# Optimization experiments

Hardware: AMD Instinct MI355X
Metric: run time of the kernel (lower is better)

Reference implementation:

```python
import jax, jax.numpy as jnp
import numpy as np

B, D_IN, T = 8, 1024, 2048
K, D_CB = 8192, 8
COMMIT = 0.005
CB_LOSS_W = 1.0
EPS = 1e-12  # F.normalize eps


def _wn(v, g):
    # torch weight_norm(dim=0) on a 1x1 Conv1d: w = g * v / ||v|| per output row
    return g[:, None] * v / jnp.linalg.norm(v, axis=1, keepdims=True)


def _l2n(x):
    return x / jnp.maximum(jnp.linalg.norm(x, axis=-1, keepdims=True), EPS)


def setup_inputs() -> dict:
    key = jax.random.key(0)
    ks = jax.random.split(key, 8)
    return {
        "z": jax.random.normal(ks[0], (B, D_IN, T), dtype=jnp.float32),
        "in_v": jax.random.normal(ks[1], (D_CB, D_IN), dtype=jnp.float32) * 0.02,
        "in_g": jnp.ones((D_CB,), dtype=jnp.float32),
        "in_b": jnp.zeros((D_CB,), dtype=jnp.float32),
        "out_v": jax.random.normal(ks[2], (D_IN, D_CB), dtype=jnp.float32) * 0.02,
        "out_g": jnp.ones((D_IN,), dtype=jnp.float32),
        "out_b": jnp.zeros((D_IN,), dtype=jnp.float32),
        "codebook": jax.random.normal(ks[3], (K, D_CB), dtype=jnp.float32),
    }


def reference(z, in_v, in_g, in_b, out_v, out_g, out_b, codebook):
    sg = jax.lax.stop_gradient
    # in_project: weight-normed 1x1 conv == matmul over channel dim
    w_in = _wn(in_v, in_g)
    z_e = jnp.einsum('oi,bit->bot', w_in, z) + in_b[None, :, None]  # [B, D_CB, T]

    # decode_latents
    enc = jnp.transpose(z_e, (0, 2, 1)).reshape(-1, D_CB)  # (B*T, D_CB)
    enc_n = _l2n(enc)
    cb_n = _l2n(codebook)
    dist = (jnp.sum(enc_n**2, axis=1, keepdims=True)
            - 2.0 * enc_n @ cb_n.T
            + jnp.sum(cb_n**2, axis=1)[None, :])  # (B*T, K)
    indices = jnp.argmin(dist, axis=1).reshape(B, T)  # [B, T]
    z_q = jnp.transpose(codebook[indices], (0, 2, 1))  # [B, D_CB, T] (unnormalized codebook)

    # training losses (per-batch means over (d, t))
    commit_loss = jnp.mean((z_e - sg(z_q)) ** 2, axis=(1, 2)) * COMMIT
    codebook_loss = jnp.mean((z_q - sg(z_e)) ** 2, axis=(1, 2)) * CB_LOSS_W

    # straight-through estimator
    z_q_st = z_e + sg(z_q - z_e)

    # out_project
    w_out = _wn(out_v, out_g)
    z_q_out = jnp.einsum('od,bdt->bot', w_out, z_q_st) + out_b[None, :, None]  # [B, D_IN, T]
    return (z_q_out, commit_loss, codebook_loss, indices, z_e)
```

## Files before the change

kernel.cpp:

```cpp
#include <hip/hip_runtime.h>
#include <math.h>
#include <stdint.h>

#define BB    8
#define DIN   1024
#define TT    2048
#define KK    8192
#define DCB   8
#define NPOS  (BB*TT)
#define KCHUNKS 64
#define KCH     (KK/KCHUNKS)
#define MARGIN  6e-4f

#define OFF_ZQOUT  0
#define OFF_COMMIT 16777216
#define OFF_CBLOSS 16777224
#define OFF_IDX    16777232
#define OFF_ZE     16793616

typedef short s8v __attribute__((ext_vector_type(8)));
typedef float f4v __attribute__((ext_vector_type(4)));

__device__ __forceinline__ unsigned short f2bf(float f) {
    unsigned u = __float_as_uint(f);
    u += 0x7FFF + ((u >> 16) & 1);
    return (unsigned short)(u >> 16);
}
__device__ __forceinline__ float bf2f(unsigned short h) {
    return __uint_as_float(((unsigned)h) << 16);
}

__global__ __launch_bounds__(256) void k_prep(
    const float* __restrict__ in_v, const float* __restrict__ in_g,
    const float* __restrict__ out_v, const float* __restrict__ out_g,
    const float* __restrict__ cb,
    float* __restrict__ w_in_f, float* __restrict__ w_out_f,
    double* __restrict__ cb_n, double* __restrict__ s_k,
    unsigned short* __restrict__ cb16, float* __restrict__ skp_f)
{
    __shared__ double red[256];
    int tid = threadIdx.x;
    int blk = blockIdx.x;

    if (blk < 8) {
        int r = blk;
        double s = 0.0;
        for (int i = tid; i < DIN; i += 256) {
            double v = (double)in_v[r*DIN + i];
            s += v*v;
        }
        red[tid] = s; __syncthreads();
        for (int off = 128; off > 0; off >>= 1) {
            if (tid < off) red[tid] += red[tid+off];
            __syncthreads();
        }
        double scale = (double)in_g[r] / sqrt(red[0]);
        for (int i = tid; i < DIN; i += 256)
            w_in_f[i*DCB + r] = (float)(scale * (double)in_v[r*DIN + i]);
    } else if (blk < 12) {
        int o = (blk-8)*256 + tid;
        float vv[DCB];
        double s = 0.0;
        #pragma unroll
        for (int d = 0; d < DCB; ++d) {
            vv[d] = out_v[o*DCB + d];
            s += (double)vv[d]*(double)vv[d];
        }
        double scale = (double)out_g[o] / sqrt(s);
        #pragma unroll
        for (int d = 0; d < DCB; ++d)
            w_out_f[o*DCB + d] = (float)(scale * (double)vv[d]);
    } else {
        int k = (blk-12)*256 + tid;
        double v[DCB]; double s = 0.0;
        #pragma unroll
        for (int d = 0; d < DCB; ++d) {
            v[d] = (double)cb[k*DCB + d];
            s += v[d]*v[d];
        }
        double nrm = sqrt(s);
        if (nrm < 1e-12) nrm = 1e-12;
        double s2 = 0.0;
        #pragma unroll
        for (int d = 0; d < DCB; ++d) {
            double t = v[d] / nrm;
            cb_n[(size_t)k*DCB + d] = t;
            s2 += t*t;
            float cf = (float)t;
            unsigned short bh = f2bf(cf);
            unsigned short bl = f2bf(cf - bf2f(bh));
            cb16[(size_t)k*16 + d]     = bh;
            cb16[(size_t)k*16 + 8 + d] = bl;
        }
        s_k[k] = s2;
        skp_f[k] = (float)(s2 + 4.0);
    }
}

__global__ __launch_bounds__(256) void k_inproj(
    const float* __restrict__ z, const float* __restrict__ w_in_f,
    const float* __restrict__ in_b,
    float* __restrict__ ze_out, double* __restrict__ enc_n,
    double* __restrict__ q_s, unsigned short* __restrict__ enc16)
{
    __shared__ float sm[DIN*DCB];

    int tid = threadIdx.x;
    {
        const uint4* src = (const uint4*)w_in_f;
        uint4* dst = (uint4*)sm;
        #pragma unroll
        for (int x = 0; x < 8; ++x) dst[tid + 256*x] = src[tid + 256*x];
    }
    __syncthreads();

    int p = tid & 7;
    int q = tid >> 3;
    int pos0 = blockIdx.x*32;
    int b = pos0 >> 11, t0 = pos0 & (TT-1);

    const float* zp = z + ((size_t)b*DIN + q)*TT + t0 + p*4;

    float acc[DCB][4];
    #pragma unroll
    for (int o = 0; o < DCB; ++o)
        #pragma unroll
        for (int j = 0; j < 4; ++j) acc[o][j] = 0.f;

    #pragma unroll
    for (int ii = 0; ii < 32; ++ii) {
        f4v zv = *(const f4v*)(zp + (size_t)ii*32*TT);
        const f4v* wp = (const f4v*)(sm + (ii*32 + q)*DCB);
        f4v w0 = wp[0], w1 = wp[1];
        #pragma unroll
        for (int j = 0; j < 4; ++j) {
            acc[0][j] += w0[0]*zv[j];
            acc[1][j] += w0[1]*zv[j];
            acc[2][j] += w0[2]*zv[j];
            acc[3][j] += w0[3]*zv[j];
            acc[4][j] += w1[0]*zv[j];
            acc[5][j] += w1[1]*zv[j];
            acc[6][j] += w1[2]*zv[j];
            acc[7][j] += w1[3]*zv[j];
        }
    }

    #pragma unroll
    for (int o = 0; o < DCB; ++o)
        #pragma unroll
        for (int j = 0; j < 4; ++j) {
            float v = acc[o][j];
            v += __shfl_xor(v, 8, 64);
            v += __shfl_xor(v, 16, 64);
            v += __shfl_xor(v, 32, 64);
            acc[o][j] = v;
        }

    __syncthreads();
    int lane = tid & 63, wv = tid >> 6;
    if ((lane >> 3) == 0) {
        float* rp = sm + wv*256 + p*32;
        #pragma unroll
        for (int o = 0; o < DCB; ++o)
            #pragma unroll
            for (int j = 0; j < 4; ++j) rp[o*4 + j] = acc[o][j];
    }
    __syncthreads();

    int o2 = tid & 7, p32 = tid >> 3;
    double s = 0.0;
    #pragma unroll
    for (int w2 = 0; w2 < 4; ++w2)
        s += (double)sm[w2*256 + (p32 >> 2)*32 + o2*4 + (p32 & 3)];
    s += (double)in_b[o2];

    int pos = pos0 + p32;
    int b3 = pos >> 11, t3 = pos & (TT-1);
    ze_out[((size_t)b3*DCB + o2)*TT + t3] = (float)s;

    double n2 = s*s;
    n2 += __shfl_xor(n2, 1, 64);
    n2 += __shfl_xor(n2, 2, 64);
    n2 += __shfl_xor(n2, 4, 64);
    double nrm = sqrt(n2);
    if (nrm < 1e-12) nrm = 1e-12;
    double e = s / nrm;
    enc_n[(size_t)pos*DCB + o2] = e;
    double s2 = e*e;
    s2 += __shfl_xor(s2, 1, 64);
    s2 += __shfl_xor(s2, 2, 64);
    s2 += __shfl_xor(s2, 4, 64);
    if (o2 == 0) q_s[pos] = s2;

    float ef = (float)(-2.0 * e);
    unsigned short ah = f2bf(ef);
    unsigned short al = f2bf(ef - bf2f(ah));
    enc16[(size_t)pos*16 + o2]     = ah;
    enc16[(size_t)pos*16 + 8 + o2] = al;
}

#define SCR_QB 64
#define SCR_CB 8
__global__ __launch_bounds__(256) void k_screen(
    const unsigned short* __restrict__ enc16,
    const unsigned short* __restrict__ cb16,
    const float* __restrict__ skp_f,
    int* __restrict__ d1key)
{
    __shared__ unsigned short cbl[SCR_CB*KCH*16];
    __shared__ float skl[SCR_CB*KCH];
    int tid = threadIdx.x;
    int cg = blockIdx.y;

    {
        const uint4* src = (const uint4*)(cb16 + (size_t)cg*SCR_CB*KCH*16);
        uint4* dst = (uint4*)cbl;
        for (int x = tid; x < SCR_CB*KCH*2; x += 256) dst[x] = src[x];
        const float* ss = skp_f + cg*SCR_CB*KCH;
        for (int x = tid; x < SCR_CB*KCH; x += 256) skl[x] = ss[x];
    }
    __syncthreads();

    int lane = tid & 63;
    int wv   = tid >> 6;
    int col  = lane & 15, quad = lane >> 4;
    int qbase = blockIdx.x*SCR_QB + wv*16;

    s8v a;
    {
        const s8v* ap = (const s8v*)(enc16 + ((size_t)(qbase + col))*16 + (quad==1 ? 8 : 0));
        a = *ap;
        if (quad == 3) { s8v zz = {0,0,0,0,0,0,0,0}; a = zz; }
    }
    int bsel = (quad == 2) ? 1 : 0;

    for (int c2 = 0; c2 < SCR_CB; ++c2) {
        int d0 = 0x7F800000, d1r = 0x7F800000, d2r = 0x7F800000, d3r = 0x7F800000;
        const s8v* bp = (const s8v*)(cbl + c2*KCH*16);
        const float* sp = skl + c2*KCH;
        #pragma unroll
        for (int t = 0; t < 8; ++t) {
            int n = t*16 + col;
            s8v bfr = bp[n*2 + bsel];
            float sk = sp[n];
            f4v acc = {sk, sk, sk, sk};
            acc = __builtin_amdgcn_mfma_f32_16x16x32_bf16(a, bfr, acc, 0, 0, 0);
            d0  = min(d0,  (int)((__float_as_uint(acc.x) & 0xFFFFFF80u) | (unsigned)n));
            d1r = min(d1r, (int)((__float_as_uint(acc.y) & 0xFFFFFF80u) | (unsigned)n));
            d2r = min(d2r, (int)((__float_as_uint(acc.z) & 0xFFFFFF80u) | (unsigned)n));
            d3r = min(d3r, (int)((__float_as_uint(acc.w) & 0xFFFFFF80u) | (unsigned)n));
        }
        #pragma unroll
        for (int off = 1; off < 16; off <<= 1) {
            d0  = min(d0,  __shfl_xor(d0,  off, 64));
            d1r = min(d1r, __shfl_xor(d1r, off, 64));
            d2r = min(d2r, __shfl_xor(d2r, off, 64));
            d3r = min(d3r, __shfl_xor(d3r, off, 64));
        }
        if (col == 0) {
            int chunk = cg*SCR_CB + c2;
            int qrow  = qbase + quad*4;
            int* dst = d1key + (size_t)qrow*KCHUNKS + chunk;
            dst[0*KCHUNKS] = d0;
            dst[1*KCHUNKS] = d1r;
            dst[2*KCHUNKS] = d2r;
            dst[3*KCHUNKS] = d3r;
        }
    }
}

__global__ __launch_bounds__(256) void k_verify(
    const int* __restrict__ d1key,
    const double* __restrict__ enc_n, const double* __restrict__ q_s,
    const double* __restrict__ cb_n, const double* __restrict__ s_k,
    const float* __restrict__ cb, const float* __restrict__ ze,
    float* __restrict__ idx_f, int* __restrict__ idx_i,
    double* __restrict__ loss_q)
{
    int tid = threadIdx.x;
    int lane = tid & 63;
    int pos = blockIdx.x*4 + (tid >> 6);

    int myk = d1key[(size_t)pos*KCHUNKS + lane];
    int m = myk;
    #pragma unroll
    for (int off = 1; off < 64; off <<= 1) m = min(m, __shfl_xor(m, off, 64));
    float thr = __int_as_float(m & 0xFFFFFF80) + MARGIN;
    bool scan = __int_as_float(myk & 0xFFFFFF80) <= thr;
    unsigned long long mask = __ballot(scan);

    double e[DCB];
    #pragma unroll
    for (int d = 0; d < DCB; ++d) e[d] = enc_n[(size_t)pos*DCB + d];
    double qs = q_s[pos];

    double bd = 1e300; int bi = 0x7FFFFFFF;
    while (mask) {
        int c = __ffsll((long long)mask) - 1;
        mask &= mask - 1;
        #pragma unroll
        for (int r = 0; r < KCH/64; ++r) {
            int k = c*KCH + r*64 + lane;
            const double* cp = cb_n + (size_t)k*DCB;
            double dot = e[0]*cp[0] + e[1]*cp[1] + e[2]*cp[2] + e[3]*cp[3]
                       + e[4]*cp[4] + e[5]*cp[5] + e[6]*cp[6] + e[7]*cp[7];
            double dist = qs - 2.0*dot + s_k[k];
            if (dist < bd || (dist == bd && k < bi)) { bd = dist; bi = k; }
        }
    }
    #pragma unroll
    for (int off = 1; off < 64; off <<= 1) {
        double od = __shfl_xor(bd, off, 64);
        int    oi = __shfl_xor(bi, off, 64);
        if (od < bd || (od == bd && oi < bi)) { bd = od; bi = oi; }
    }
    if (lane == 0) {
        int b = pos >> 11, t = pos & (TT-1);
        idx_f[pos] = (float)bi;
        idx_i[pos] = bi;
        double ssum = 0.0;
        #pragma unroll
        for (int d = 0; d < DCB; ++d) {
            double zev = (double)ze[((size_t)b*DCB + d)*TT + t];
            double zqv = (double)cb[bi*DCB + d];
            double diff = zev - zqv;
            ssum += diff*diff;
        }
        loss_q[pos] = ssum;
    }
}

__global__ __launch_bounds__(256) void k_losses(
    const double* __restrict__ loss_q,
    float* __restrict__ commit_out, float* __restrict__ cbloss_out)
{
    __shared__ double red[256];
    int tid = threadIdx.x;
    int b = blockIdx.x;
    double s = 0.0;
    for (int i = tid; i < TT; i += 256) s += loss_q[(size_t)b*TT + i];
    red[tid] = s; __syncthreads();
    for (int off = 128; off > 0; off >>= 1) {
        if (tid < off) red[tid] += red[tid+off];
        __syncthreads();
    }
    if (tid == 0) {
        double m = red[0] / (double)(DCB*TT);
        commit_out[b] = (float)(m * 0.005);
        cbloss_out[b] = (float)m;
    }
}

__global__ __launch_bounds__(256) void k_out_proj(
    const float* __restrict__ cb, const float* __restrict__ ze,
    const int* __restrict__ idx_i, const float* __restrict__ w_out,
    const float* __restrict__ out_b, float* __restrict__ zq_out)
{
    __shared__ float wl[128*DCB];
    __shared__ float bl[128];
    int tid = threadIdx.x;

    int oc = blockIdx.y;
    int obase = oc*128;
    for (int x = tid; x < 128*DCB; x += 256) wl[x] = w_out[obase*DCB + x];
    for (int x = tid; x < 128; x += 256) bl[x] = out_b[obase + x];
    __syncthreads();

    int pos = blockIdx.x*256 + tid;
    int b = pos >> 11, t = pos & (TT-1);
    int ki = idx_i[pos];
    float zq[DCB];
    #pragma unroll
    for (int d = 0; d < DCB; ++d) {
        float zev = ze[((size_t)b*DCB + d)*TT + t];
        float zqv = cb[ki*DCB + d];
        zq[d] = zev + (zqv - zev);
    }
    float* outp = zq_out + ((size_t)b*DIN + obase)*TT + t;
    for (int oo = 0; oo < 128; ++oo) {
        float acc = 0.f;
        #pragma unroll
        for (int d = 0; d < DCB; ++d) acc += wl[oo*DCB + d]*zq[d];
        acc += bl[oo];
        outp[(size_t)oo*TT] = acc;
    }
}

extern "C" void kernel_launch(void* const* d_in, const int* in_sizes, int n_in,
                              void* d_out, int out_size, void* d_ws, size_t ws_size,
                              hipStream_t stream)
{
    const float* z        = (const float*)d_in[0];
    const float* in_v     = (const float*)d_in[1];
    const float* in_g     = (const float*)d_in[2];
    const float* in_b     = (const float*)d_in[3];
    const float* out_v    = (const float*)d_in[4];
    const float* out_g    = (const float*)d_in[5];
    const float* out_b    = (const float*)d_in[6];
    const float* codebook = (const float*)d_in[7];

    float* out = (float*)d_out;
    float* zq_out_p  = out + OFF_ZQOUT;
    float* commit_p  = out + OFF_COMMIT;
    float* cbloss_p  = out + OFF_CBLOSS;
    float* idx_p     = out + OFF_IDX;
    float* ze_p      = out + OFF_ZE;

    float*  w_in_f = (float*)d_ws;
    double* cb_n   = (double*)d_ws + DCB*DIN;
    double* s_k    = cb_n + (size_t)KK*DCB;
    double* enc_n  = s_k + KK;
    double* q_s    = enc_n + (size_t)NPOS*DCB;
    double* loss_q = q_s + NPOS;
    float*  w_out  = (float*)(loss_q + NPOS);
    float*  skp_f  = w_out + DCB*DIN;
    unsigned short* cb16  = (unsigned short*)(skp_f + KK);
    unsigned short* enc16 = cb16 + (size_t)KK*16;
    int*    d1key  = (int*)(enc16 + (size_t)NPOS*16);
    int*    idx_i  = d1key + (size_t)NPOS*KCHUNKS;

    k_prep<<<44, 256, 0, stream>>>(in_v, in_g, out_v, out_g, codebook,
                                   w_in_f, w_out, cb_n, s_k, cb16, skp_f);
    k_inproj<<<NPOS/32, 256, 0, stream>>>(z, w_in_f, in_b, ze_p, enc_n, q_s, enc16);
    k_screen<<<dim3(NPOS/SCR_QB, KCHUNKS/SCR_CB), 256, 0, stream>>>(
        enc16, cb16, skp_f, d1key);
    k_verify<<<NPOS/4, 256, 0, stream>>>(d1key, enc_n, q_s, cb_n, s_k,
                                         codebook, ze_p, idx_p, idx_i, loss_q);
    k_losses<<<BB, 256, 0, stream>>>(loss_q, commit_p, cbloss_p);
    k_out_proj<<<dim3(NPOS/256, DIN/128), 256, 0, stream>>>(
        codebook, ze_p, idx_i, w_out, out_b, zq_out_p);
}
```

Measured before the change: 185.8 us.

## Fuse loss reduction into verify via atomics, drop screen key masking, halve out-proj tile

Removes the separate k_losses launch. k_verify now reduces per-block loss partials in shared memory and atomically adds them into a small zeroed accumulator, and the first k_out_proj block finalizes the per-batch means. The screen kernel stops masking the low mantissa bits before OR-ing in the index, which saves an AND per candidate but lets index bits perturb the packed distance key slightly. k_out_proj now covers 64 output channels per block instead of 128, giving twice as many blocks. The loss sums now depend on atomic ordering and are no longer deterministic.

```diff
diff --git a/kernel.cpp b/kernel.cpp
--- a/kernel.cpp
+++ b/kernel.cpp
@@ -36,13 +36,15 @@
     const float* __restrict__ cb,
     float* __restrict__ w_in_f, float* __restrict__ w_out_f,
     double* __restrict__ cb_n, double* __restrict__ s_k,
-    unsigned short* __restrict__ cb16, float* __restrict__ skp_f)
+    unsigned short* __restrict__ cb16, float* __restrict__ skp_f,
+    double* __restrict__ lacc)
 {
     __shared__ double red[256];
     int tid = threadIdx.x;
     int blk = blockIdx.x;
 
     if (blk < 8) {
+        if (blk == 0 && tid < 64) lacc[tid] = 0.0;
         int r = blk;
         double s = 0.0;
         for (int i = tid; i < DIN; i += 256) {
@@ -245,10 +247,10 @@
             float sk = sp[n];
             f4v acc = {sk, sk, sk, sk};
             acc = __builtin_amdgcn_mfma_f32_16x16x32_bf16(a, bfr, acc, 0, 0, 0);
-            d0  = min(d0,  (int)((__float_as_uint(acc.x) & 0xFFFFFF80u) | (unsigned)n));
-            d1r = min(d1r, (int)((__float_as_uint(acc.y) & 0xFFFFFF80u) | (unsigned)n));
-            d2r = min(d2r, (int)((__float_as_uint(acc.z) & 0xFFFFFF80u) | (unsigned)n));
-            d3r = min(d3r, (int)((__float_as_uint(acc.w) & 0xFFFFFF80u) | (unsigned)n));
+            d0  = min(d0,  (int)(__float_as_uint(acc.x) | (unsigned)n));
+            d1r = min(d1r, (int)(__float_as_uint(acc.y) | (unsigned)n));
+            d2r = min(d2r, (int)(__float_as_uint(acc.z) | (unsigned)n));
+            d3r = min(d3r, (int)(__float_as_uint(acc.w) | (unsigned)n));
         }
         #pragma unroll
         for (int off = 1; off < 16; off <<= 1) {
@@ -275,11 +277,13 @@
     const double* __restrict__ cb_n, const double* __restrict__ s_k,
     const float* __restrict__ cb, const float* __restrict__ ze,
     float* __restrict__ idx_f, int* __restrict__ idx_i,
-    double* __restrict__ loss_q)
-{
+    double* __restrict__ lacc)
+{
+    __shared__ double sred[4];
     int tid = threadIdx.x;
     int lane = tid & 63;
-    int pos = blockIdx.x*4 + (tid >> 6);
+    int wv = tid >> 6;
+    int pos = blockIdx.x*4 + wv;
 
     int myk = d1key[(size_t)pos*KCHUNKS + lane];
     int m = myk;
@@ -326,44 +330,40 @@
             double diff = zev - zqv;
             ssum += diff*diff;
         }
-        loss_q[pos] = ssum;
-    }
-}
-
-__global__ __launch_bounds__(256) void k_losses(
-    const double* __restrict__ loss_q,
-    float* __restrict__ commit_out, float* __restrict__ cbloss_out)
-{
-    __shared__ double red[256];
-    int tid = threadIdx.x;
-    int b = blockIdx.x;
-    double s = 0.0;
-    for (int i = tid; i < TT; i += 256) s += loss_q[(size_t)b*TT + i];
-    red[tid] = s; __syncthreads();
-    for (int off = 128; off > 0; off >>= 1) {
-        if (tid < off) red[tid] += red[tid+off];
-        __syncthreads();
-    }
+        sred[wv] = ssum;
+    }
+    __syncthreads();
     if (tid == 0) {
-        double m = red[0] / (double)(DCB*TT);
-        commit_out[b] = (float)(m * 0.005);
-        cbloss_out[b] = (float)m;
+        double t4 = sred[0] + sred[1] + sred[2] + sred[3];
+        int b = (blockIdx.x*4) >> 11;
+        atomicAdd(&lacc[b*8 + (blockIdx.x & 7)], t4);
     }
 }
 
 __global__ __launch_bounds__(256) void k_out_proj(
     const float* __restrict__ cb, const float* __restrict__ ze,
     const int* __restrict__ idx_i, const float* __restrict__ w_out,
-    const float* __restrict__ out_b, float* __restrict__ zq_out)
-{
-    __shared__ float wl[128*DCB];
-    __shared__ float bl[128];
+    const float* __restrict__ out_b, const double* __restrict__ lacc,
+    float* __restrict__ commit_out, float* __restrict__ cbloss_out,
+    float* __restrict__ zq_out)
+{
+    __shared__ float wl[64*DCB];
+    __shared__ float bl[64];
     int tid = threadIdx.x;
 
+    if (blockIdx.x == 0 && blockIdx.y == 0 && tid < 8) {
+        double s = 0.0;
+        #pragma unroll
+        for (int j = 0; j < 8; ++j) s += lacc[tid*8 + j];
+        double mm = s / (double)(DCB*TT);
+        commit_out[tid] = (float)(mm * 0.005);
+        cbloss_out[tid] = (float)mm;
+    }
+
     int oc = blockIdx.y;
-    int obase = oc*128;
-    for (int x = tid; x < 128*DCB; x += 256) wl[x] = w_out[obase*DCB + x];
-    for (int x = tid; x < 128; x += 256) bl[x] = out_b[obase + x];
+    int obase = oc*64;
+    for (int x = tid; x < 64*DCB; x += 256) wl[x] = w_out[obase*DCB + x];
+    if (tid < 64) bl[tid] = out_b[obase + tid];
     __syncthreads();
 
     int pos = blockIdx.x*256 + tid;
@@ -377,7 +377,7 @@
         zq[d] = zev + (zqv - zev);
     }
     float* outp = zq_out + ((size_t)b*DIN + obase)*TT + t;
-    for (int oo = 0; oo < 128; ++oo) {
+    for (int oo = 0; oo < 64; ++oo) {
         float acc = 0.f;
         #pragma unroll
         for (int d = 0; d < DCB; ++d) acc += wl[oo*DCB + d]*zq[d];
@@ -418,15 +418,15 @@
     unsigned short* enc16 = cb16 + (size_t)KK*16;
     int*    d1key  = (int*)(enc16 + (size_t)NPOS*16);
     int*    idx_i  = d1key + (size_t)NPOS*KCHUNKS;
+    double* lacc   = (double*)(idx_i + NPOS);
 
     k_prep<<<44, 256, 0, stream>>>(in_v, in_g, out_v, out_g, codebook,
-                                   w_in_f, w_out, cb_n, s_k, cb16, skp_f);
+                                   w_in_f, w_out, cb_n, s_k, cb16, skp_f, lacc);
     k_inproj<<<NPOS/32, 256, 0, stream>>>(z, w_in_f, in_b, ze_p, enc_n, q_s, enc16);
     k_screen<<<dim3(NPOS/SCR_QB, KCHUNKS/SCR_CB), 256, 0, stream>>>(
         enc16, cb16, skp_f, d1key);
     k_verify<<<NPOS/4, 256, 0, stream>>>(d1key, enc_n, q_s, cb_n, s_k,
-                                         codebook, ze_p, idx_p, idx_i, loss_q);
-    k_losses<<<BB, 256, 0, stream>>>(loss_q, commit_p, cbloss_p);
-    k_out_proj<<<dim3(NPOS/256, DIN/128), 256, 0, stream>>>(
-        codebook, ze_p, idx_i, w_out, out_b, zq_out_p);
-}
+                                         codebook, ze_p, idx_p, idx_i, lacc);
+    k_out_proj<<<dim3(NPOS/256, DIN/64), 256, 0, stream>>>(
+        codebook, ze_p, idx_i, w_out, out_b, lacc, commit_p, cbloss_p, zq_out_p);
+}
```

Result: slower. 190.4 us (+2.5%).
